# Performance work log

Measured on AMD Instinct MI355X. Metric: run time of the kernel, lower is better.

## Reference

```python
import jax, jax.numpy as jnp
import numpy as np
from jax import lax

B, H, D, S, T, V = 128, 512, 512, 80, 28, 30000

def setup_inputs() -> dict:
    key = jax.random.key(0)
    ks = jax.random.split(key, 20)
    s = 0.02
    return {
        "encoder_last_hidden_state": jax.random.normal(ks[0], (1, B, H), jnp.float32),
        "encoder_output": jax.random.normal(ks[1], (B, S, H), jnp.float32),
        "targets": jax.random.randint(ks[2], (B, T), 0, V),
        "embedding": jax.random.normal(ks[3], (V, D), jnp.float32) * s,
        "W1": jax.random.normal(ks[4], (H, 2 * H), jnp.float32) * s,
        "b1": jnp.zeros((H,), jnp.float32),
        "W2": jax.random.normal(ks[5], (H, H), jnp.float32) * s,
        "b2": jnp.zeros((H,), jnp.float32),
        "W3": jax.random.normal(ks[6], (H, H), jnp.float32) * s,
        "b3": jnp.zeros((H,), jnp.float32),
        "W4": jax.random.normal(ks[7], (H, H), jnp.float32) * s,
        "b4": jnp.zeros((H,), jnp.float32),
        "w_att": jax.random.normal(ks[8], (1, H), jnp.float32) * s,
        "W_ih": jax.random.normal(ks[9], (4 * H, H + D), jnp.float32) * s,
        "W_hh": jax.random.normal(ks[10], (4 * H, H), jnp.float32) * s,
        "b_ih": jnp.zeros((4 * H,), jnp.float32),
        "b_hh": jnp.zeros((4 * H,), jnp.float32),
        "W_out": jax.random.normal(ks[11], (V, H), jnp.float32) * s,
        "b_out": jnp.zeros((V,), jnp.float32),
    }


def reference(encoder_last_hidden_state, encoder_output, targets, embedding,
              W1, b1, W2, b2, W3, b3, W4, b4, w_att,
              W_ih, W_hh, b_ih, b_hh, W_out, b_out):
    # Deterministic teacher forcing (threshold > max of random.uniform for large tr_steps).
    h = encoder_last_hidden_state[0]          # (B, H)
    c = jnp.zeros_like(h)
    emb = embedding[targets[:, :-1]]          # (B, T-1, D)
    xs = jnp.swapaxes(emb, 0, 1)              # (T-1, B, D)

    def step(carry, x):
        h, c = carry
        # --- attention (4 stacked linears, no nonlinearity, as in source) ---
        hs = jnp.broadcast_to(h[:, None, :], encoder_output.shape)  # (B,S,H)
        m = jnp.concatenate([encoder_output, hs], axis=-1)          # (B,S,2H)
        a = m @ W1.T + b1
        a = a @ W2.T + b2
        a = a @ W3.T + b3
        a = a @ W4.T + b4
        scores = jnp.einsum('bsh,h->bs', a, w_att[0])               # (B,S)
        att = jax.nn.softmax(scores, axis=1)
        ctx = jnp.einsum('bs,bsh->bh', att, encoder_output)         # (B,H)
        # --- single-step LSTM (PyTorch gate order i,f,g,o) ---
        li = jnp.concatenate([x, ctx], axis=-1)                     # (B, D+H)
        gates = li @ W_ih.T + h @ W_hh.T + b_ih + b_hh
        i_, f_, g_, o_ = jnp.split(gates, 4, axis=-1)
        c2 = jax.nn.sigmoid(f_) * c + jax.nn.sigmoid(i_) * jnp.tanh(g_)
        h2 = jax.nn.sigmoid(o_) * jnp.tanh(c2)
        logits = h2 @ W_out.T + b_out                               # (B,V)
        return (h2, c2), logits

    _, logits = lax.scan(step, (h, c), xs)    # (T-1, B, V)
    seq_logProb = jnp.swapaxes(logits, 0, 1)  # (B, T-1, V)
    seq_predictions = jnp.argmax(seq_logProb, axis=-1)
    return seq_logProb, seq_predictions
```

## Files before the change

kernel.cpp:

```cpp
#include <hip/hip_runtime.h>
#include <math.h>

#define BB 128
#define HH 512
#define SS 80
#define NT 27
#define VV 30000
#define NBLK 469

typedef short bf16x8 __attribute__((ext_vector_type(8)));
typedef float f32x4  __attribute__((ext_vector_type(4)));
typedef unsigned long long u64;

#define OFF_WE     0
#define OFF_CTX    512
#define OFF_H      (OFF_CTX + BB*HH)
#define OFF_C      (OFF_H + BB*HH)
#define OFF_GATES  (OFF_C + BB*HH)
#define OFF_SLOTS  (OFF_GATES + BB*2048)
#define OFF_GCTX   (OFF_SLOTS + 2*NT*BB)
#define OFF_GIN    (OFF_GCTX + BB*2048)
#define WS_FULL_FLOATS (OFF_GIN + NT*BB*2048)
#define OFF_WHI    WS_FULL_FLOATS
#define OFF_WLO    (OFF_WHI + VV*256)
#define OFF_HHI    (OFF_WLO + VV*256)
#define OFF_HLO    (OFF_HHI + BB*256)
#define OFF_PART   (OFF_HLO + BB*256)
#define WS_MFMA_FLOATS (OFF_PART + NT*NBLK*BB*2)
#define OFF_WHI_B   WS_FULL_FLOATS
#define OFF_WLO_B   (OFF_WHI_B + VV*256)
#define OFF_HALLHI  (OFF_WLO_B + VV*256)
#define OFF_HALLLO  (OFF_HALLHI + NT*BB*256)
#define OFF_PART_B  (OFF_HALLLO + NT*BB*256)
#define WS_BATCH_FLOATS (OFF_PART_B + NT*NBLK*BB*2)

__device__ __forceinline__ unsigned long long pack_max(float v, int n) {
    unsigned u = __float_as_uint(v);
    unsigned key = (u & 0x80000000u) ? ~u : (u | 0x80000000u);
    return ((unsigned long long)key << 32) | (unsigned)(~(unsigned)n);
}

__device__ __forceinline__ unsigned short bf16_rne(float x) {
    unsigned u = __float_as_uint(x);
    unsigned r = (u + 0x7fffu + ((u >> 16) & 1u)) >> 16;
    return (unsigned short)r;
}
__device__ __forceinline__ float bf16f(unsigned short h) {
    return __uint_as_float((unsigned)h << 16);
}
__device__ __forceinline__ u64 shfl_xor_u64(u64 v, int m) {
    unsigned lo = (unsigned)v, hi = (unsigned)(v >> 32);
    lo = __shfl_xor(lo, m, 64);
    hi = __shfl_xor(hi, m, 64);
    return ((u64)hi << 32) | lo;
}

__global__ void k_init(const float* __restrict__ elhs, float* __restrict__ h,
                       float* __restrict__ c, unsigned long long* __restrict__ slots) {
    int i = blockIdx.x * blockDim.x + threadIdx.x;
    if (i < BB * HH) { h[i] = elhs[i]; c[i] = 0.f; }
    if (i < NT * BB) slots[i] = 0ull;
}

__global__ __launch_bounds__(256) void k_we(const float* __restrict__ W1, const float* __restrict__ W2,
                                            const float* __restrict__ W3, const float* __restrict__ W4,
                                            const float* __restrict__ watt, float* __restrict__ we_out) {
    __shared__ float v[HH], v2[HH];
    int tid = threadIdx.x;
    for (int k = tid; k < HH; k += 256) v[k] = watt[k];
    __syncthreads();
    const float* Ws[3] = {W4, W3, W2};
    for (int l = 0; l < 3; ++l) {
        const float* W = Ws[l];
        for (int k = tid; k < HH; k += 256) {
            float s = 0.f;
            for (int j = 0; j < HH; ++j) s += v[j] * W[j * HH + k];
            v2[k] = s;
        }
        __syncthreads();
        for (int k = tid; k < HH; k += 256) v[k] = v2[k];
        __syncthreads();
    }
    for (int k = tid; k < HH; k += 256) {
        float s = 0.f;
        for (int j = 0; j < HH; ++j) s += v[j] * W1[j * (2 * HH) + k];
        we_out[k] = s;
    }
}

__global__ __launch_bounds__(256) void k_attn(const float* __restrict__ eo, const float* __restrict__ we,
                                              float* __restrict__ ctx) {
    __shared__ float wsm[HH];
    __shared__ float sc[SS];
    int b = blockIdx.x, tid = threadIdx.x;
    for (int k = tid; k < HH; k += 256) wsm[k] = we[k];
    __syncthreads();
    int wid = tid >> 6, lane = tid & 63;
    const float* eob = eo + (size_t)b * SS * HH;
    for (int s = wid; s < SS; s += 4) {
        float p = 0.f;
        for (int k = lane; k < HH; k += 64) p += eob[s * HH + k] * wsm[k];
        for (int off = 32; off > 0; off >>= 1) p += __shfl_down(p, off, 64);
        if (lane == 0) sc[s] = p;
    }
    __syncthreads();
    if (wid == 0) {
        float a = (lane < SS) ? sc[lane] : -INFINITY;
        float bv = (lane + 64 < SS) ? sc[lane + 64] : -INFINITY;
        float m = fmaxf(a, bv);
        for (int off = 32; off > 0; off >>= 1) m = fmaxf(m, __shfl_down(m, off, 64));
        m = __shfl(m, 0, 64);
        float e0 = (lane < SS) ? expf(a - m) : 0.f;
        float e1 = (lane + 64 < SS) ? expf(bv - m) : 0.f;
        float ssum = e0 + e1;
        for (int off = 32; off > 0; off >>= 1) ssum += __shfl_down(ssum, off, 64);
        ssum = __shfl(ssum, 0, 64);
        float inv = 1.f / ssum;
        if (lane < SS) sc[lane] = e0 * inv;
        if (lane + 64 < SS) sc[lane + 64] = e1 * inv;
    }
    __syncthreads();
    for (int hh = tid; hh < HH; hh += 256) {
        float acc = 0.f;
        for (int s = 0; s < SS; ++s) acc += sc[s] * eob[s * HH + hh];
        ctx[b * HH + hh] = acc;
    }
}

__global__ __launch_bounds__(256) void k_gin(const float* __restrict__ emb, const int* __restrict__ targets,
                                             const float* __restrict__ Wih, float* __restrict__ gin) {
    const int n0 = blockIdx.x * 64, m0 = blockIdx.y * 64;
    __shared__ __align__(16) float As[32][68];
    __shared__ __align__(16) float Bs[32][68];
    int tid = threadIdx.x;
    int tx = tid & 15, ty = tid >> 4;
    float acc[4][4] = {};
    for (int kt = 0; kt < 512; kt += 32) {
        #pragma unroll
        for (int i = 0; i < 2; ++i) {
            int idx = tid + i * 256;
            int mm = idx >> 3, k4 = (idx & 7) * 4;
            int m = m0 + mm;
            int t = m >> 7, b = m & 127;
            int row = targets[b * 28 + t];
            float4 v = *(const float4*)(emb + (size_t)row * 512 + kt + k4);
            As[k4 + 0][mm] = v.x; As[k4 + 1][mm] = v.y; As[k4 + 2][mm] = v.z; As[k4 + 3][mm] = v.w;
        }
        #pragma unroll
        for (int i = 0; i < 2; ++i) {
            int idx = tid + i * 256;
            int nn = idx >> 3, k4 = (idx & 7) * 4;
            float4 v = *(const float4*)(Wih + (size_t)(n0 + nn) * 1024 + kt + k4);
            Bs[k4 + 0][nn] = v.x; Bs[k4 + 1][nn] = v.y; Bs[k4 + 2][nn] = v.z; Bs[k4 + 3][nn] = v.w;
        }
        __syncthreads();
        #pragma unroll
        for (int k = 0; k < 32; ++k) {
            float4 a = *(const float4*)&As[k][ty * 4];
            float4 b4 = *(const float4*)&Bs[k][tx * 4];
            float av[4] = {a.x, a.y, a.z, a.w}, bv[4] = {b4.x, b4.y, b4.z, b4.w};
            #pragma unroll
            for (int i = 0; i < 4; ++i)
                #pragma unroll
                for (int j = 0; j < 4; ++j) acc[i][j] += av[i] * bv[j];
        }
        __syncthreads();
    }
    #pragma unroll
    for (int i = 0; i < 4; ++i) {
        int m = m0 + ty * 4 + i;
        float4 o = {acc[i][0], acc[i][1], acc[i][2], acc[i][3]};
        *(float4*)(gin + (size_t)m * 2048 + n0 + tx * 4) = o;
    }
}

__global__ __launch_bounds__(256) void k_gctx(const float* __restrict__ ctx, const float* __restrict__ Wih,
                                              const float* __restrict__ bih, const float* __restrict__ bhh,
                                              float* __restrict__ gctx) {
    const int n0 = blockIdx.x * 64, m0 = blockIdx.y * 32;
    __shared__ __align__(16) float As[32][36];
    __shared__ __align__(16) float Bs[32][68];
    int tid = threadIdx.x;
    int tx = tid & 15, ty = tid >> 4;
    float acc[2][4] = {};
    for (int kt = 0; kt < 512; kt += 32) {
        {
            int mm = tid >> 3, k4 = (tid & 7) * 4;
            float4 v = *(const float4*)(ctx + (size_t)(m0 + mm) * 512 + kt + k4);
            As[k4 + 0][mm] = v.x; As[k4 + 1][mm] = v.y; As[k4 + 2][mm] = v.z; As[k4 + 3][mm] = v.w;
        }
        #pragma unroll
        for (int i = 0; i < 2; ++i) {
            int idx = tid + i * 256;
            int nn = idx >> 3, k4 = (idx & 7) * 4;
            float4 v = *(const float4*)(Wih + (size_t)(n0 + nn) * 1024 + 512 + kt + k4);
            Bs[k4 + 0][nn] = v.x; Bs[k4 + 1][nn] = v.y; Bs[k4 + 2][nn] = v.z; Bs[k4 + 3][nn] = v.w;
        }
        __syncthreads();
        #pragma unroll
        for (int k = 0; k < 32; ++k) {
            float a0 = As[k][ty * 2], a1 = As[k][ty * 2 + 1];
            float4 b4 = *(const float4*)&Bs[k][tx * 4];
            float bv[4] = {b4.x, b4.y, b4.z, b4.w};
            #pragma unroll
            for (int j = 0; j < 4; ++j) { acc[0][j] += a0 * bv[j]; acc[1][j] += a1 * bv[j]; }
        }
        __syncthreads();
    }
    #pragma unroll
    for (int i = 0; i < 2; ++i) {
        int b = m0 + ty * 2 + i;
        int n = n0 + tx * 4;
        float4 o = {acc[i][0] + bih[n] + bhh[n], acc[i][1] + bih[n + 1] + bhh[n + 1],
                    acc[i][2] + bih[n + 2] + bhh[n + 2], acc[i][3] + bih[n + 3] + bhh[n + 3]};
        *(float4*)(gctx + (size_t)b * 2048 + n) = o;
    }
}

template <bool FULL>
__global__ __launch_bounds__(256) void k_gates(const float* __restrict__ emb, const int* __restrict__ targets,
                                               const float* __restrict__ ctx, const float* __restrict__ h,
                                               const float* __restrict__ Wih, const float* __restrict__ Whh,
                                               const float* __restrict__ bih, const float* __restrict__ bhh,
                                               const float* __restrict__ gin, const float* __restrict__ gctx,
                                               float* __restrict__ gates, int t) {
    const int n0 = blockIdx.x * 64, m0 = blockIdx.y * 32;
    __shared__ __align__(16) float As[32][36];
    __shared__ __align__(16) float Bs[32][68];
    int tid = threadIdx.x;
    int tx = tid & 15, ty = tid >> 4;
    float acc[2][4] = {};
    const int KTOT = FULL ? 1536 : 512;
    for (int kt = 0; kt < KTOT; kt += 32) {
        {
            int mm = tid >> 3, k4 = (tid & 7) * 4;
            int b = m0 + mm, k = kt + k4;
            const float* src;
            if (FULL) {
                if (k < 512) { int row = targets[b * 28 + t]; src = emb + (size_t)row * 512 + k; }
                else if (k < 1024) src = ctx + (size_t)b * 512 + (k - 512);
                else src = h + (size_t)b * 512 + (k - 1024);
            } else {
                src = h + (size_t)b * 512 + k;
            }
            float4 v = *(const float4*)src;
            As[k4 + 0][mm] = v.x; As[k4 + 1][mm] = v.y; As[k4 + 2][mm] = v.z; As[k4 + 3][mm] = v.w;
        }
        #pragma unroll
        for (int i = 0; i < 2; ++i) {
            int idx = tid + i * 256;
            int nn = idx >> 3, k4 = (idx & 7) * 4;
            int n = n0 + nn, k = kt + k4;
            const float* src;
            if (FULL) {
                if (k < 1024) src = Wih + (size_t)n * 1024 + k;
                else src = Whh + (size_t)n * 512 + (k - 1024);
            } else {
                src = Whh + (size_t)n * 512 + k;
            }
            float4 v = *(const float4*)src;
            Bs[k4 + 0][nn] = v.x; Bs[k4 + 1][nn] = v.y; Bs[k4 + 2][nn] = v.z; Bs[k4 + 3][nn] = v.w;
        }
        __syncthreads();
        #pragma unroll
        for (int k = 0; k < 32; ++k) {
            float a0 = As[k][ty * 2], a1 = As[k][ty * 2 + 1];
            float4 b4 = *(const float4*)&Bs[k][tx * 4];
            float bv[4] = {b4.x, b4.y, b4.z, b4.w};
            #pragma unroll
            for (int j = 0; j < 4; ++j) { acc[0][j] += a0 * bv[j]; acc[1][j] += a1 * bv[j]; }
        }
        __syncthreads();
    }
    #pragma unroll
    for (int i = 0; i < 2; ++i) {
        int b = m0 + ty * 2 + i;
        int n = n0 + tx * 4;
        float base[4];
        if (FULL) {
            #pragma unroll
            for (int j = 0; j < 4; ++j) base[j] = bih[n + j] + bhh[n + j];
        } else {
            const float* g1 = gin + ((size_t)t * BB + b) * 2048 + n;
            const float* g2 = gctx + (size_t)b * 2048 + n;
            #pragma unroll
            for (int j = 0; j < 4; ++j) base[j] = g1[j] + g2[j];
        }
        float4 o = {acc[i][0] + base[0], acc[i][1] + base[1], acc[i][2] + base[2], acc[i][3] + base[3]};
        *(float4*)(gates + (size_t)b * 2048 + n) = o;
    }
}

__global__ void k_lstm(const float* __restrict__ gates, float* __restrict__ h, float* __restrict__ c) {
    int idx = blockIdx.x * blockDim.x + threadIdx.x;
    int b = idx >> 9, j = idx & 511;
    const float* g = gates + (size_t)b * 2048;
    float iv = g[j], fv = g[512 + j], gv = g[1024 + j], ov = g[1536 + j];
    float si = 1.f / (1.f + expf(-iv));
    float sf = 1.f / (1.f + expf(-fv));
    float so = 1.f / (1.f + expf(-ov));
    float c2 = sf * c[idx] + si * tanhf(gv);
    c[idx] = c2;
    h[idx] = so * tanhf(c2);
}

__global__ void k_lstm2(const float* __restrict__ gates, float* __restrict__ h, float* __restrict__ c,
                        unsigned short* __restrict__ hHi, unsigned short* __restrict__ hLo) {
    int idx = blockIdx.x * blockDim.x + threadIdx.x;
    int b = idx >> 9, j = idx & 511;
    const float* g = gates + (size_t)b * 2048;
    float iv = g[j], fv = g[512 + j], gv = g[1024 + j], ov = g[1536 + j];
    float si = 1.f / (1.f + expf(-iv));
    float sf = 1.f / (1.f + expf(-fv));
    float so = 1.f / (1.f + expf(-ov));
    float c2 = sf * c[idx] + si * tanhf(gv);
    c[idx] = c2;
    float hv = so * tanhf(c2);
    h[idx] = hv;
    unsigned short hh = bf16_rne(hv);
    hHi[idx] = hh;
    hLo[idx] = bf16_rne(hv - bf16f(hh));
}

__global__ __launch_bounds__(256) void k_split(const float* __restrict__ src, unsigned short* __restrict__ hi,
                                               unsigned short* __restrict__ lo, int n4) {
    int i = blockIdx.x * 256 + threadIdx.x;
    if (i >= n4) return;
    float4 v = ((const float4*)src)[i];
    unsigned short h0 = bf16_rne(v.x), h1 = bf16_rne(v.y), h2 = bf16_rne(v.z), h3 = bf16_rne(v.w);
    ushort4 hv = {h0, h1, h2, h3};
    ushort4 lv = {bf16_rne(v.x - bf16f(h0)), bf16_rne(v.y - bf16f(h1)),
                  bf16_rne(v.z - bf16f(h2)), bf16_rne(v.w - bf16f(h3))};
    ((ushort4*)hi)[i] = hv;
    ((ushort4*)lo)[i] = lv;
}

__global__ __launch_bounds__(256, 3) void k_vprojB(
    const unsigned short* __restrict__ hAllHi, const unsigned short* __restrict__ hAllLo,
    const unsigned short* __restrict__ wHi, const unsigned short* __restrict__ wLo,
    const float* __restrict__ bout, float* __restrict__ out,
    u64* __restrict__ part)
{
    const int bid = blockIdx.x;
    const int nblk = bid / NT;
    const int t = bid - nblk * NT;
    const int n0 = nblk * 64;
    const int tid = threadIdx.x;
    const int lane = tid & 63;
    const int wv = tid >> 6;
    const int g = lane >> 4;
    const int q = lane & 15;

    int aIdx[2];
    int bIdx[4], colv[4];
    float bo[4];
    #pragma unroll
    for (int mt = 0; mt < 2; ++mt)
        aIdx[mt] = ((t * BB) + wv * 32 + mt * 16 + q) * 512 + g * 8;
    #pragma unroll
    for (int nt = 0; nt < 4; ++nt) {
        int col = n0 + nt * 16 + q;
        colv[nt] = col;
        int cc = col < VV ? col : (VV - 1);
        bIdx[nt] = cc * 512 + g * 8;
        bo[nt] = bout[cc];
    }

    f32x4 zero = {0.f, 0.f, 0.f, 0.f};
    f32x4 acc[2][4];
    #pragma unroll
    for (int mt = 0; mt < 2; ++mt)
        #pragma unroll
        for (int nt = 0; nt < 4; ++nt) acc[mt][nt] = zero;

    for (int s = 0; s < 16; ++s) {
        const int K = s * 32;
        bf16x8 aH[2], aL[2], bH[4], bL[4];
        #pragma unroll
        for (int mt = 0; mt < 2; ++mt) {
            aH[mt] = *(const bf16x8*)(hAllHi + aIdx[mt] + K);
            aL[mt] = *(const bf16x8*)(hAllLo + aIdx[mt] + K);
        }
        #pragma unroll
        for (int nt = 0; nt < 4; ++nt) {
            bH[nt] = *(const bf16x8*)(wHi + bIdx[nt] + K);
            bL[nt] = *(const bf16x8*)(wLo + bIdx[nt] + K);
        }
        #pragma unroll
        for (int mt = 0; mt < 2; ++mt)
            #pragma unroll
            for (int nt = 0; nt < 4; ++nt) {
                acc[mt][nt] = __builtin_amdgcn_mfma_f32_16x16x32_bf16(aH[mt], bH[nt], acc[mt][nt], 0, 0, 0);
                acc[mt][nt] = __builtin_amdgcn_mfma_f32_16x16x32_bf16(aH[mt], bL[nt], acc[mt][nt], 0, 0, 0);
                acc[mt][nt] = __builtin_amdgcn_mfma_f32_16x16x32_bf16(aL[mt], bH[nt], acc[mt][nt], 0, 0, 0);
            }
    }

    #pragma unroll
    for (int mt = 0; mt < 2; ++mt) {
        #pragma unroll
        for (int r = 0; r < 4; ++r) {
            int row = wv * 32 + mt * 16 + 4 * g + r;
            u64 pk = 0ull;
            #pragma unroll
            for (int nt = 0; nt < 4; ++nt) {
                float v = acc[mt][nt][r] + bo[nt];
                int col = colv[nt];
                if (col < VV) out[((size_t)row * NT + t) * VV + col] = v;
                u64 p2 = pack_max(v, col);
                if (p2 > pk) pk = p2;
            }
            #pragma unroll
            for (int m_ = 1; m_ < 16; m_ <<= 1) {
                u64 o = shfl_xor_u64(pk, m_);
                if (o > pk) pk = o;
            }
            if (q == 0) part[((size_t)t * NBLK + nblk) * BB + row] = pk;
        }
    }
}

__global__ __launch_bounds__(256, 2) void k_vproj2(
    const unsigned short* __restrict__ hHi, const unsigned short* __restrict__ hLo,
    const unsigned short* __restrict__ wHi, const unsigned short* __restrict__ wLo,
    const float* __restrict__ bout, float* __restrict__ out,
    u64* __restrict__ part, int t)
{
    const int tid = threadIdx.x;
    const int lane = tid & 63;
    const int wv = tid >> 6;
    const int wm = wv >> 1;
    const int wn = wv & 1;
    const int g = lane >> 4;
    const int q = lane & 15;
    const int n0 = blockIdx.x * 64;

    int aIdx[4];
    int bIdx[2], colv[2];
    float bo[2];
    #pragma unroll
    for (int mt = 0; mt < 4; ++mt) aIdx[mt] = (wm * 64 + mt * 16 + q) * 512 + g * 8;
    #pragma unroll
    for (int nt = 0; nt < 2; ++nt) {
        int col = n0 + wn * 32 + nt * 16 + q;
        colv[nt] = col;
        int cc = col < VV ? col : (VV - 1);
        bIdx[nt] = cc * 512 + g * 8;
        bo[nt] = bout[cc];
    }

    f32x4 zero = {0.f, 0.f, 0.f, 0.f};
    f32x4 acc[4][2];
    #pragma unroll
    for (int mt = 0; mt < 4; ++mt)
        #pragma unroll
        for (int nt = 0; nt < 2; ++nt) acc[mt][nt] = zero;

    for (int s = 0; s < 16; ++s) {
        const int K = s * 32;
        bf16x8 aH[4], aL[4], bH[2], bL[2];
        #pragma unroll
        for (int mt = 0; mt < 4; ++mt) {
            aH[mt] = *(const bf16x8*)(hHi + aIdx[mt] + K);
            aL[mt] = *(const bf16x8*)(hLo + aIdx[mt] + K);
        }
        #pragma unroll
        for (int nt = 0; nt < 2; ++nt) {
            bH[nt] = *(const bf16x8*)(wHi + bIdx[nt] + K);
            bL[nt] = *(const bf16x8*)(wLo + bIdx[nt] + K);
        }
        #pragma unroll
        for (int mt = 0; mt < 4; ++mt)
            #pragma unroll
            for (int nt = 0; nt < 2; ++nt) {
                acc[mt][nt] = __builtin_amdgcn_mfma_f32_16x16x32_bf16(aH[mt], bH[nt], acc[mt][nt], 0, 0, 0);
                acc[mt][nt] = __builtin_amdgcn_mfma_f32_16x16x32_bf16(aH[mt], bL[nt], acc[mt][nt], 0, 0, 0);
                acc[mt][nt] = __builtin_amdgcn_mfma_f32_16x16x32_bf16(aL[mt], bH[nt], acc[mt][nt], 0, 0, 0);
            }
    }

    __shared__ u64 red[BB][2];
    #pragma unroll
    for (int mt = 0; mt < 4; ++mt) {
        #pragma unroll
        for (int r = 0; r < 4; ++r) {
            int row = wm * 64 + mt * 16 + 4 * g + r;
            u64 pk = 0ull;
            #pragma unroll
            for (int nt = 0; nt < 2; ++nt) {
                float v = acc[mt][nt][r] + bo[nt];
                int col = colv[nt];
                if (col < VV) out[((size_t)row * NT + t) * VV + col] = v;
                u64 p2 = pack_max(v, col);
                if (p2 > pk) pk = p2;
            }
            #pragma unroll
            for (int m_ = 1; m_ < 16; m_ <<= 1) {
                u64 o = shfl_xor_u64(pk, m_);
                if (o > pk) pk = o;
            }
            if (q == 0) red[row][wn] = pk;
        }
    }
    __syncthreads();
    if (tid < BB) {
        u64 a = red[tid][0], b2 = red[tid][1];
        part[((size_t)t * NBLK + blockIdx.x) * BB + tid] = a > b2 ? a : b2;
    }
}

__global__ __launch_bounds__(256) void k_vproj(const float* __restrict__ h, const float* __restrict__ Wout,
                                               const float* __restrict__ bout, float* __restrict__ out,
                                               unsigned long long* __restrict__ slots, int t) {
    const int n0 = blockIdx.x * 64, m0 = blockIdx.y * 64;
    __shared__ __align__(16) float As[32][68];
    __shared__ __align__(16) float Bs[32][68];
    __shared__ unsigned long long red[64][17];
    int tid = threadIdx.x;
    int tx = tid & 15, ty = tid >> 4;
    float acc[4][4] = {};
    for (int kt = 0; kt < 512; kt += 32) {
        #pragma unroll
        for (int i = 0; i < 2; ++i) {
            int idx = tid + i * 256;
            int mm = idx >> 3, k4 = (idx & 7) * 4;
            float4 v = *(const float4*)(h + (size_t)(m0 + mm) * 512 + kt + k4);
            As[k4 + 0][mm] = v.x; As[k4 + 1][mm] = v.y; As[k4 + 2][mm] = v.z; As[k4 + 3][mm] = v.w;
        }
        #pragma unroll
        for (int i = 0; i < 2; ++i) {
            int idx = tid + i * 256;
            int nn = idx >> 3, k4 = (idx & 7) * 4;
            int n = n0 + nn; if (n >= VV) n = VV - 1;
            float4 v = *(const float4*)(Wout + (size_t)n * 512 + kt + k4);
            Bs[k4 + 0][nn] = v.x; Bs[k4 + 1][nn] = v.y; Bs[k4 + 2][nn] = v.z; Bs[k4 + 3][nn] = v.w;
        }
        __syncthreads();
        #pragma unroll
        for (int k = 0; k < 32; ++k) {
            float4 a = *(const float4*)&As[k][ty * 4];
            float4 b4 = *(const float4*)&Bs[k][tx * 4];
            float av[4] = {a.x, a.y, a.z, a.w}, bv[4] = {b4.x, b4.y, b4.z, b4.w};
            #pragma unroll
            for (int i = 0; i < 4; ++i)
                #pragma unroll
                for (int j = 0; j < 4; ++j) acc[i][j] += av[i] * bv[j];
        }
        __syncthreads();
    }
    #pragma unroll
    for (int i = 0; i < 4; ++i) {
        int m = m0 + ty * 4 + i;
        int n = n0 + tx * 4;
        float vals[4];
        #pragma unroll
        for (int j = 0; j < 4; ++j) vals[j] = acc[i][j] + ((n + j < VV) ? bout[n + j] : 0.f);
        size_t ob = ((size_t)m * NT + t) * VV;
        if (n + 3 < VV) {
            float4 o = {vals[0], vals[1], vals[2], vals[3]};
            *(float4*)(out + ob + n) = o;
        } else {
            for (int j = 0; j < 4; ++j) if (n + j < VV) out[ob + n + j] = vals[j];
        }
        unsigned long long p = 0ull;
        #pragma unroll
        for (int j = 0; j < 4; ++j)
            if (n + j < VV) {
                unsigned long long pk = pack_max(vals[j], n + j);
                if (pk > p) p = pk;
            }
        red[ty * 4 + i][tx] = p;
    }
    __syncthreads();
    if (tid < 64) {
        unsigned long long best = red[tid][0];
        #pragma unroll
        for (int j = 1; j < 16; ++j) { unsigned long long q = red[tid][j]; if (q > best) best = q; }
        atomicMax(&slots[t * BB + (m0 + tid)], best);
    }
}

__global__ void k_final(const unsigned long long* __restrict__ slots, float* __restrict__ out) {
    int i = blockIdx.x * blockDim.x + threadIdx.x;
    if (i >= NT * BB) return;
    int t = i / BB, b = i % BB;
    unsigned idx = ~(unsigned)(slots[i] & 0xffffffffull);
    out[(size_t)BB * NT * VV + (size_t)b * NT + t] = (float)idx;
}

__global__ void k_final2(const u64* __restrict__ part, float* __restrict__ out) {
    int i = blockIdx.x * blockDim.x + threadIdx.x;
    if (i >= NT * BB) return;
    int t = i >> 7, b = i & 127;
    const u64* p = part + (size_t)t * NBLK * BB + b;
    u64 best = 0ull;
    for (int nb = 0; nb < NBLK; ++nb) {
        u64 v = p[(size_t)nb * BB];
        if (v > best) best = v;
    }
    unsigned idx = ~(unsigned)(best & 0xffffffffull);
    out[(size_t)BB * NT * VV + (size_t)b * NT + t] = (float)idx;
}

extern "C" void kernel_launch(void* const* d_in, const int* in_sizes, int n_in,
                              void* d_out, int out_size, void* d_ws, size_t ws_size,
                              hipStream_t stream) {
    const float* elhs    = (const float*)d_in[0];
    const float* eo      = (const float*)d_in[1];
    const int*   targets = (const int*)d_in[2];
    const float* emb     = (const float*)d_in[3];
    const float* W1      = (const float*)d_in[4];
    const float* W2      = (const float*)d_in[6];
    const float* W3      = (const float*)d_in[8];
    const float* W4      = (const float*)d_in[10];
    const float* watt    = (const float*)d_in[12];
    const float* Wih     = (const float*)d_in[13];
    const float* Whh     = (const float*)d_in[14];
    const float* bih     = (const float*)d_in[15];
    const float* bhh     = (const float*)d_in[16];
    const float* Wout    = (const float*)d_in[17];
    const float* bout    = (const float*)d_in[18];

    float* out = (float*)d_out;
    float* ws  = (float*)d_ws;
    float* we    = ws + OFF_WE;
    float* ctx   = ws + OFF_CTX;
    float* h     = ws + OFF_H;
    float* c     = ws + OFF_C;
    float* gates = ws + OFF_GATES;
    unsigned long long* slots = (unsigned long long*)(ws + OFF_SLOTS);
    float* gctx  = ws + OFF_GCTX;
    float* gin   = ws + OFF_GIN;

    const bool use_gin   = ws_size >= (size_t)WS_FULL_FLOATS * sizeof(float);
    const bool use_batch = ws_size >= (size_t)WS_BATCH_FLOATS * sizeof(float);
    const bool use_mfma  = !use_batch && ws_size >= (size_t)WS_MFMA_FLOATS * sizeof(float);

    k_init<<<256, 256, 0, stream>>>(elhs, h, c, slots);
    k_we<<<1, 256, 0, stream>>>(W1, W2, W3, W4, watt, we);
    k_attn<<<BB, 256, 0, stream>>>(eo, we, ctx);
    if (use_gin) {
        k_gin<<<dim3(32, 54), 256, 0, stream>>>(emb, targets, Wih, gin);
        k_gctx<<<dim3(32, 4), 256, 0, stream>>>(ctx, Wih, bih, bhh, gctx);
    }

    if (use_batch) {
        unsigned short* wHi    = (unsigned short*)(ws + OFF_WHI_B);
        unsigned short* wLo    = (unsigned short*)(ws + OFF_WLO_B);
        unsigned short* hAllHi = (unsigned short*)(ws + OFF_HALLHI);
        unsigned short* hAllLo = (unsigned short*)(ws + OFF_HALLLO);
        u64* part = (u64*)(ws + OFF_PART_B);
        k_split<<<(VV * 128 + 255) / 256, 256, 0, stream>>>(Wout, wHi, wLo, VV * 128);
        for (int t = 0; t < NT; ++t) {
            if (use_gin)
                k_gates<false><<<dim3(32, 4), 256, 0, stream>>>(emb, targets, ctx, h, Wih, Whh, bih, bhh, gin, gctx, gates, t);
            else
                k_gates<true><<<dim3(32, 4), 256, 0, stream>>>(emb, targets, ctx, h, Wih, Whh, bih, bhh, gin, gctx, gates, t);
            k_lstm2<<<128, 512, 0, stream>>>(gates, h, c,
                                             hAllHi + (size_t)t * BB * 512,
                                             hAllLo + (size_t)t * BB * 512);
        }
        k_vprojB<<<NBLK * NT, 256, 0, stream>>>(hAllHi, hAllLo, wHi, wLo, bout, out, part);
        k_final2<<<14, 256, 0, stream>>>(part, out);
    } else if (use_mfma) {
        unsigned short* wHi = (unsigned short*)(ws + OFF_WHI);
        unsigned short* wLo = (unsigned short*)(ws + OFF_WLO);
        unsigned short* hHi = (unsigned short*)(ws + OFF_HHI);
        unsigned short* hLo = (unsigned short*)(ws + OFF_HLO);
        u64* part = (u64*)(ws + OFF_PART);
        k_split<<<(VV * 128 + 255) / 256, 256, 0, stream>>>(Wout, wHi, wLo, VV * 128);
        for (int t = 0; t < NT; ++t) {
            if (use_gin)
                k_gates<false><<<dim3(32, 4), 256, 0, stream>>>(emb, targets, ctx, h, Wih, Whh, bih, bhh, gin, gctx, gates, t);
            else
                k_gates<true><<<dim3(32, 4), 256, 0, stream>>>(emb, targets, ctx, h, Wih, Whh, bih, bhh, gin, gctx, gates, t);
            k_lstm2<<<128, 512, 0, stream>>>(gates, h, c, hHi, hLo);
            k_vproj2<<<NBLK, 256, 0, stream>>>(hHi, hLo, wHi, wLo, bout, out, part, t);
        }
        k_final2<<<14, 256, 0, stream>>>(part, out);
    } else {
        for (int t = 0; t < NT; ++t) {
            if (use_gin)
                k_gates<false><<<dim3(32, 4), 256, 0, stream>>>(emb, targets, ctx, h, Wih, Whh, bih, bhh, gin, gctx, gates, t);
            else
                k_gates<true><<<dim3(32, 4), 256, 0, stream>>>(emb, targets, ctx, h, Wih, Whh, bih, bhh, gin, gctx, gates, t);
            k_lstm<<<128, 512, 0, stream>>>(gates, h, c);
            k_vproj<<<dim3(469, 2), 256, 0, stream>>>(h, Wout, bout, out, slots, t);
        }
        k_final<<<14, 256, 0, stream>>>(slots, out);
    }
}
```

Measured before the change: 2.526 ms.

## Parallelize attention weight-chain matvecs and swizzle vocab projection block order

```diff
diff --git a/kernel.cpp b/kernel.cpp
--- a/kernel.cpp
+++ b/kernel.cpp
@@ -62,30 +62,25 @@
     if (i < NT * BB) slots[i] = 0ull;
 }
 
-__global__ __launch_bounds__(256) void k_we(const float* __restrict__ W1, const float* __restrict__ W2,
-                                            const float* __restrict__ W3, const float* __restrict__ W4,
-                                            const float* __restrict__ watt, float* __restrict__ we_out) {
-    __shared__ float v[HH], v2[HH];
+__global__ __launch_bounds__(256) void k_matvecT(const float* __restrict__ W, int ld,
+                                                 const float* __restrict__ vin,
+                                                 float* __restrict__ vout) {
+    __shared__ float vs[HH];
+    __shared__ float red[4][64];
     int tid = threadIdx.x;
-    for (int k = tid; k < HH; k += 256) v[k] = watt[k];
+    for (int j = tid; j < HH; j += 256) vs[j] = vin[j];
     __syncthreads();
-    const float* Ws[3] = {W4, W3, W2};
-    for (int l = 0; l < 3; ++l) {
-        const float* W = Ws[l];
-        for (int k = tid; k < HH; k += 256) {
-            float s = 0.f;
-            for (int j = 0; j < HH; ++j) s += v[j] * W[j * HH + k];
-            v2[k] = s;
-        }
-        __syncthreads();
-        for (int k = tid; k < HH; k += 256) v[k] = v2[k];
-        __syncthreads();
-    }
-    for (int k = tid; k < HH; k += 256) {
-        float s = 0.f;
-        for (int j = 0; j < HH; ++j) s += v[j] * W1[j * (2 * HH) + k];
-        we_out[k] = s;
-    }
+    int c  = tid & 63;
+    int jg = tid >> 6;
+    int k  = blockIdx.x * 64 + c;
+    float s = 0.f;
+    #pragma unroll 4
+    for (int j = jg * 128; j < jg * 128 + 128; ++j)
+        s += vs[j] * W[(size_t)j * ld + k];
+    red[jg][c] = s;
+    __syncthreads();
+    if (tid < 64)
+        vout[blockIdx.x * 64 + tid] = red[0][tid] + red[1][tid] + red[2][tid] + red[3][tid];
 }
 
 __global__ __launch_bounds__(256) void k_attn(const float* __restrict__ eo, const float* __restrict__ we,
@@ -335,15 +330,19 @@
     ((ushort4*)lo)[i] = lv;
 }
 
-__global__ __launch_bounds__(256, 3) void k_vprojB(
+__global__ __launch_bounds__(256, 5) void k_vprojB(
     const unsigned short* __restrict__ hAllHi, const unsigned short* __restrict__ hAllLo,
     const unsigned short* __restrict__ wHi, const unsigned short* __restrict__ wLo,
     const float* __restrict__ bout, float* __restrict__ out,
     u64* __restrict__ part)
 {
     const int bid = blockIdx.x;
-    const int nblk = bid / NT;
-    const int t = bid - nblk * NT;
+    const int x = bid & 7;
+    const int r = bid >> 3;
+    const int g2 = r / NT;
+    const int t = r - g2 * NT;
+    const int nblk = g2 * 8 + x;
+    if (nblk >= NBLK) return;
     const int n0 = nblk * 64;
     const int tid = threadIdx.x;
     const int lane = tid & 63;
@@ -399,12 +398,12 @@
     #pragma unroll
     for (int mt = 0; mt < 2; ++mt) {
         #pragma unroll
-        for (int r = 0; r < 4; ++r) {
-            int row = wv * 32 + mt * 16 + 4 * g + r;
+        for (int rr = 0; rr < 4; ++rr) {
+            int row = wv * 32 + mt * 16 + 4 * g + rr;
             u64 pk = 0ull;
             #pragma unroll
             for (int nt = 0; nt < 4; ++nt) {
-                float v = acc[mt][nt][r] + bo[nt];
+                float v = acc[mt][nt][rr] + bo[nt];
                 int col = colv[nt];
                 if (col < VV) out[((size_t)row * NT + t) * VV + col] = v;
                 u64 p2 = pack_max(v, col);
@@ -483,12 +482,12 @@
     #pragma unroll
     for (int mt = 0; mt < 4; ++mt) {
         #pragma unroll
-        for (int r = 0; r < 4; ++r) {
-            int row = wm * 64 + mt * 16 + 4 * g + r;
+        for (int rr = 0; rr < 4; ++rr) {
+            int row = wm * 64 + mt * 16 + 4 * g + rr;
             u64 pk = 0ull;
             #pragma unroll
             for (int nt = 0; nt < 2; ++nt) {
-                float v = acc[mt][nt][r] + bo[nt];
+                float v = acc[mt][nt][rr] + bo[nt];
                 int col = colv[nt];
                 if (col < VV) out[((size_t)row * NT + t) * VV + col] = v;
                 u64 p2 = pack_max(v, col);
@@ -637,7 +636,13 @@
     const bool use_mfma  = !use_batch && ws_size >= (size_t)WS_MFMA_FLOATS * sizeof(float);
 
     k_init<<<256, 256, 0, stream>>>(elhs, h, c, slots);
-    k_we<<<1, 256, 0, stream>>>(W1, W2, W3, W4, watt, we);
+    {
+        float* vtmp = gates;
+        k_matvecT<<<8, 256, 0, stream>>>(W4, HH, watt, vtmp);
+        k_matvecT<<<8, 256, 0, stream>>>(W3, HH, vtmp, we);
+        k_matvecT<<<8, 256, 0, stream>>>(W2, HH, we, vtmp);
+        k_matvecT<<<8, 256, 0, stream>>>(W1, 2 * HH, vtmp, we);
+    }
     k_attn<<<BB, 256, 0, stream>>>(eo, we, ctx);
     if (use_gin) {
         k_gin<<<dim3(32, 54), 256, 0, stream>>>(emb, targets, Wih, gin);
@@ -660,7 +665,7 @@
                                              hAllHi + (size_t)t * BB * 512,
                                              hAllLo + (size_t)t * BB * 512);
         }
-        k_vprojB<<<NBLK * NT, 256, 0, stream>>>(hAllHi, hAllLo, wHi, wLo, bout, out, part);
+        k_vprojB<<<8 * 59 * NT, 256, 0, stream>>>(hAllHi, hAllLo, wHi, wLo, bout, out, part);
         k_final2<<<14, 256, 0, stream>>>(part, out);
     } else if (use_mfma) {
         unsigned short* wHi = (unsigned short*)(ws + OFF_WHI);
```

Result: faster. 2.465 ms (-2.4%).
